# Kernel tuning notes

Measured on AMD Instinct MI355X. Metric: run time of the kernel, lower is better.

The kernel has to match this reference:

```python
import jax, jax.numpy as jnp
import numpy as np

B, S, DIM, H, FFN = 2, 2048, 1024, 16, 4096
HD = DIM // H
THETA = 10000.0
EPS = 1e-5


def setup_inputs() -> dict:
    key = jax.random.key(0)
    ks = jax.random.split(key, 12)
    s = 0.02
    return {
        "x": jax.random.normal(ks[0], (B, S, DIM), jnp.float32),
        "padding_mask": jnp.zeros((B, S), jnp.bool_),
        "qkv_w": jax.random.normal(ks[1], (DIM, 3 * DIM), jnp.float32) * s,
        "qkv_b": jnp.zeros((3 * DIM,), jnp.float32),
        "out_w": jax.random.normal(ks[2], (DIM, DIM), jnp.float32) * s,
        "out_b": jnp.zeros((DIM,), jnp.float32),
        "ln1_g": jnp.ones((DIM,), jnp.float32),
        "ln1_b": jnp.zeros((DIM,), jnp.float32),
        "ln2_g": jnp.ones((DIM,), jnp.float32),
        "ln2_b": jnp.zeros((DIM,), jnp.float32),
        "w1": jax.random.normal(ks[3], (DIM, FFN), jnp.float32) * s,
        "b1": jnp.zeros((FFN,), jnp.float32),
        "w2": jax.random.normal(ks[4], (FFN, DIM), jnp.float32) * s,
        "b2": jnp.zeros((DIM,), jnp.float32),
    }


def _layer_norm(x, g, b):
    mu = jnp.mean(x, axis=-1, keepdims=True)
    var = jnp.mean(jnp.square(x - mu), axis=-1, keepdims=True)
    return (x - mu) * jax.lax.rsqrt(var + EPS) * g + b


def _rotate_half(x):
    x1, x2 = jnp.split(x, 2, axis=-1)
    return jnp.concatenate([-x2, x1], axis=-1)


def reference(x, padding_mask, qkv_w, qkv_b, out_w, out_b,
              ln1_g, ln1_b, ln2_g, ln2_b, w1, b1, w2, b2):
    b, s, _ = x.shape
    residual = x
    h = _layer_norm(x, ln1_g, ln1_b)
    qkv = h @ qkv_w + qkv_b  # [b, s, 3*dim]
    q, k, v = jnp.split(qkv, 3, axis=-1)
    # [b, heads, s, head_dim]
    q = q.reshape(b, s, H, HD).transpose(0, 2, 1, 3)
    k = k.reshape(b, s, H, HD).transpose(0, 2, 1, 3)
    v = v.reshape(b, s, H, HD).transpose(0, 2, 1, 3)

    # rotary embeddings
    pos = jnp.arange(s, dtype=jnp.float32)
    inv_freq = 1.0 / (THETA ** (jnp.arange(0, HD, 2, dtype=jnp.float32) / HD))
    freqs = pos[:, None] * inv_freq[None, :]          # [s, hd/2]
    emb = jnp.concatenate([freqs, freqs], axis=-1)    # [s, hd]
    sin = jnp.sin(emb)[None, None, :, :]
    cos = jnp.cos(emb)[None, None, :, :]
    q = q * cos + _rotate_half(q) * sin
    k = k * cos + _rotate_half(k) * sin

    scale = HD ** (-0.5)
    scores = jnp.einsum('bhqd,bhkd->bhqk', q, k) * scale
    neg = jnp.finfo(scores.dtype).min
    scores = jnp.where(padding_mask[:, None, None, :], neg, scores)
    probs = jax.nn.softmax(scores, axis=-1)
    ctx = jnp.einsum('bhqk,bhkd->bhqd', probs, v)
    ctx = ctx.transpose(0, 2, 1, 3).reshape(b, s, DIM)
    x = residual + (ctx @ out_w + out_b)

    residual = x
    h = _layer_norm(x, ln2_g, ln2_b)
    h = jax.nn.gelu(h @ w1 + b1, approximate=False) @ w2 + b2
    return residual + h
```

## Files before the change

kernel.cpp:

```cpp
#include <hip/hip_runtime.h>
#include <hip/hip_bf16.h>
#include <math.h>

typedef __hip_bfloat16 bf16;
typedef __attribute__((ext_vector_type(8))) short short8;
typedef __attribute__((ext_vector_type(4))) float floatx4;

constexpr int BB   = 2;
constexpr int SS   = 2048;
constexpr int DIMc = 1024;
constexpr int Hc   = 16;
constexpr int HDc  = 64;
constexpr int FFNc = 4096;
constexpr int TOK  = BB * SS;
constexpr float EPSc = 1e-5f;

typedef __attribute__((address_space(1))) void gvoid;
typedef __attribute__((address_space(3))) void lvoid;
__device__ __forceinline__ void lds16(const void* g, void* l) {
    __builtin_amdgcn_global_load_lds((gvoid*)g, (lvoid*)l, 16, 0, 0);
}
__device__ __forceinline__ float fexp2(float x) { return __builtin_amdgcn_exp2f(x); }

__device__ __forceinline__ float fast_gelu(float x) {
    float x2 = x * x;
    float z = 0.7978845608028654f * x * __builtin_fmaf(0.044715f, x2, 1.0f);
    float e = fexp2(-2.885390081777927f * z);
    return x * __builtin_amdgcn_rcpf(1.0f + e);
}

__global__ __launch_bounds__(256) void ln_kernel(const float* __restrict__ x,
                                                 const float* __restrict__ g,
                                                 const float* __restrict__ b,
                                                 bf16* __restrict__ out) {
    int t = blockIdx.x;
    int tid = threadIdx.x;
    float4 v = ((const float4*)(x + (size_t)t * DIMc))[tid];
    float s  = v.x + v.y + v.z + v.w;
    float sq = v.x*v.x + v.y*v.y + v.z*v.z + v.w*v.w;
    for (int off = 1; off < 64; off <<= 1) {
        s  += __shfl_xor(s,  off, 64);
        sq += __shfl_xor(sq, off, 64);
    }
    __shared__ float ss[4], ssq[4];
    int wave = tid >> 6;
    if ((tid & 63) == 0) { ss[wave] = s; ssq[wave] = sq; }
    __syncthreads();
    s  = ss[0] + ss[1] + ss[2] + ss[3];
    sq = ssq[0] + ssq[1] + ssq[2] + ssq[3];
    float mu  = s * (1.0f / DIMc);
    float var = sq * (1.0f / DIMc) - mu * mu;
    float inv = rsqrtf(var + EPSc);
    float4 gg = ((const float4*)g)[tid];
    float4 bb = ((const float4*)b)[tid];
    size_t base = (size_t)t * DIMc + tid * 4;
    out[base + 0] = __float2bfloat16((v.x - mu) * inv * gg.x + bb.x);
    out[base + 1] = __float2bfloat16((v.y - mu) * inv * gg.y + bb.y);
    out[base + 2] = __float2bfloat16((v.z - mu) * inv * gg.z + bb.z);
    out[base + 3] = __float2bfloat16((v.w - mu) * inv * gg.w + bb.w);
}

__global__ __launch_bounds__(256) void reduce_ln_kernel(const float* __restrict__ P,
                                                        const float* __restrict__ x,
                                                        const float* __restrict__ bias,
                                                        const float* __restrict__ g,
                                                        const float* __restrict__ b,
                                                        float* __restrict__ out,
                                                        bf16* __restrict__ hout) {
    int t = blockIdx.x;
    int tid = threadIdx.x;
    size_t off = (size_t)t * DIMc / 4 + tid;
    float4 v  = ((const float4*)x)[off];
    float4 p0 = ((const float4*)P)[off];
    float4 p1 = ((const float4*)P)[off + (size_t)TOK * DIMc / 4];
    float4 bv = ((const float4*)bias)[tid];
    v.x += p0.x + p1.x + bv.x;
    v.y += p0.y + p1.y + bv.y;
    v.z += p0.z + p1.z + bv.z;
    v.w += p0.w + p1.w + bv.w;
    ((float4*)out)[off] = v;

    float s  = v.x + v.y + v.z + v.w;
    float sq = v.x*v.x + v.y*v.y + v.z*v.z + v.w*v.w;
    for (int o = 1; o < 64; o <<= 1) {
        s  += __shfl_xor(s,  o, 64);
        sq += __shfl_xor(sq, o, 64);
    }
    __shared__ float ss[4], ssq[4];
    int wave = tid >> 6;
    if ((tid & 63) == 0) { ss[wave] = s; ssq[wave] = sq; }
    __syncthreads();
    s  = ss[0] + ss[1] + ss[2] + ss[3];
    sq = ssq[0] + ssq[1] + ssq[2] + ssq[3];
    float mu  = s * (1.0f / DIMc);
    float var = sq * (1.0f / DIMc) - mu * mu;
    float inv = rsqrtf(var + EPSc);
    float4 gg = ((const float4*)g)[tid];
    float4 bb = ((const float4*)b)[tid];
    size_t base = (size_t)t * DIMc + tid * 4;
    hout[base + 0] = __float2bfloat16((v.x - mu) * inv * gg.x + bb.x);
    hout[base + 1] = __float2bfloat16((v.y - mu) * inv * gg.y + bb.y);
    hout[base + 2] = __float2bfloat16((v.z - mu) * inv * gg.z + bb.z);
    hout[base + 3] = __float2bfloat16((v.w - mu) * inv * gg.w + bb.w);
}

__global__ __launch_bounds__(256) void reduce_add_kernel(const float* __restrict__ P,
                                                         const float* __restrict__ bias,
                                                         float* __restrict__ out) {
    size_t f = (size_t)blockIdx.x * 256 + threadIdx.x;
    float4 v  = ((float4*)out)[f];
    float4 p0 = ((const float4*)P)[f];
    float4 p1 = ((const float4*)P)[f + (size_t)TOK * DIMc / 4];
    float4 bv = ((const float4*)bias)[f & (DIMc / 4 - 1)];
    v.x += p0.x + p1.x + bv.x;
    v.y += p0.y + p1.y + bv.y;
    v.z += p0.z + p1.z + bv.z;
    v.w += p0.w + p1.w + bv.w;
    ((float4*)out)[f] = v;
}

__global__ __launch_bounds__(256) void transpose_bf16(const float* __restrict__ in,
                                                      bf16* __restrict__ out,
                                                      int K, int N) {
    __shared__ float t[32][33];
    int k0 = blockIdx.y * 32, n0 = blockIdx.x * 32;
    int x = threadIdx.x & 31;
    int y = threadIdx.x >> 5;
#pragma unroll
    for (int i = 0; i < 4; ++i) {
        int k = y + i * 8;
        t[k][x] = in[(size_t)(k0 + k) * N + n0 + x];
    }
    __syncthreads();
#pragma unroll
    for (int i = 0; i < 4; ++i) {
        int n = y + i * 8;
        out[(size_t)(n0 + n) * K + k0 + x] = __float2bfloat16(t[x][n]);
    }
}

__global__ __launch_bounds__(256) void transpose_v(const bf16* __restrict__ qkv,
                                                   bf16* __restrict__ vT) {
    __shared__ short t[64][72];
    const int s0 = blockIdx.x * 64, h = blockIdx.y, b = blockIdx.z;
    const int tid = threadIdx.x;
    const short* qs = (const short*)qkv;
#pragma unroll
    for (int it = 0; it < 2; ++it) {
        int idx = it * 256 + tid;
        int r = idx >> 3, c = (idx & 7) * 8;
        *(short8*)&t[r][c] = *(const short8*)(qs + (size_t)(b * SS + s0 + r) * 3072
                                              + 2048 + h * 64 + c);
    }
    __syncthreads();
#pragma unroll
    for (int it = 0; it < 2; ++it) {
        int idx = it * 256 + tid;
        int d = idx >> 3, cs = (idx & 7) * 8;
        short8 v;
#pragma unroll
        for (int j = 0; j < 8; ++j) v[j] = t[cs + j][d];
        *(short8*)((short*)vT + ((size_t)(b * Hc + h) * 64 + d) * SS + s0 + cs) = v;
    }
}

__device__ __forceinline__ void xcd_remap(int& bx, int& by) {
    const int gn = gridDim.x;
    int lin = blockIdx.y * gn + blockIdx.x;
    int k8 = lin & 7, idx = lin >> 3;
    int hn = gn >> 1;
    by = (k8 >> 1) * 8 + (idx & 7);
    bx = (k8 & 1) * hn + (idx >> 3);
}

template <int ACT, bool ROPE>
__global__ __launch_bounds__(256) void gemm_bt(const bf16* __restrict__ A,
                                               const bf16* __restrict__ Bt,
                                               const float* __restrict__ bias,
                                               bf16* __restrict__ Cout,
                                               int M, int N, int K) {
    constexpr int BK = 64;
    __shared__ bf16 As[2][128 * 32];
    __shared__ bf16 Bs[2][128 * 32];
    const int tid = threadIdx.x;
    const int wave = tid >> 6, lane = tid & 63;
    const int lane15 = lane & 15, lgrp = lane >> 4;
    const int wm = (wave >> 1) * 64, wn = (wave & 1) * 64;
    int bx, by; xcd_remap(bx, by);
    const int row0 = by * 128, col0 = bx * 128;

    floatx4 acc[4][4] = {};

    const int srow = wave * 16 + (lane >> 2);
    const int scol = (((lane & 3) + (srow >> 1)) & 3) * 8;
    const bf16* ga = A  + (size_t)(row0 + srow) * K + scol;
    const bf16* gb = Bt + (size_t)(col0 + srow) * K + scol;
    const int g_l = (lgrp - (lane15 >> 1)) & 3;

    for (int k0 = 0; k0 < K; k0 += BK) {
        __syncthreads();
#pragma unroll
        for (int p = 0; p < 4; ++p) {
            const size_t go = (size_t)((p & 1) * 64) * K + k0 + (p >> 1) * 32;
            lds16(ga + go, &As[p >> 1][(p & 1) * 2048 + wave * 512]);
            lds16(gb + go, &Bs[p >> 1][(p & 1) * 2048 + wave * 512]);
        }
        __syncthreads();
#pragma unroll
        for (int s = 0; s < 2; ++s) {
            short8 af[4], bfr[4];
#pragma unroll
            for (int i = 0; i < 4; ++i)
                af[i] = *(const short8*)(&As[s][(wm + i * 16 + lane15) * 32 + g_l * 8]);
#pragma unroll
            for (int j = 0; j < 4; ++j)
                bfr[j] = *(const short8*)(&Bs[s][(wn + j * 16 + lane15) * 32 + g_l * 8]);
#pragma unroll
            for (int i = 0; i < 4; ++i)
#pragma unroll
                for (int j = 0; j < 4; ++j)
                    acc[i][j] = __builtin_amdgcn_mfma_f32_16x16x32_bf16(af[i], bfr[j], acc[i][j], 0, 0, 0);
        }
    }

    const bool doRope = ROPE && (col0 < 2048);
    float invf0 = 0.f, invf1 = 0.f;
    if (ROPE) {
        invf0 = fexp2(-0.4152410118609203f * (float)lane15);
        invf1 = fexp2(-0.4152410118609203f * (float)(16 + lane15));
    }
    float bv[4];
#pragma unroll
    for (int j = 0; j < 4; ++j) bv[j] = bias[col0 + wn + j * 16 + lane15];

#pragma unroll
    for (int i = 0; i < 4; ++i) {
#pragma unroll
        for (int r = 0; r < 4; ++r) {
            int row = row0 + wm + i * 16 + lgrp * 4 + r;
            float v[4];
#pragma unroll
            for (int j = 0; j < 4; ++j) v[j] = acc[i][j][r] + bv[j];
            if (doRope) {
                float pos = (float)(row & (SS - 1));
                float s0, c0, s1, c1;
                __sincosf(pos * invf0, &s0, &c0);
                __sincosf(pos * invf1, &s1, &c1);
                float t0 = v[0] * c0 - v[2] * s0;
                float t1 = v[1] * c1 - v[3] * s1;
                float t2 = v[2] * c0 + v[0] * s0;
                float t3 = v[3] * c1 + v[1] * s1;
                v[0] = t0; v[1] = t1; v[2] = t2; v[3] = t3;
            }
#pragma unroll
            for (int j = 0; j < 4; ++j) {
                float o = v[j];
                if (ACT == 1) o = fast_gelu(o);
                Cout[(size_t)row * N + col0 + wn + j * 16 + lane15] = __float2bfloat16(o);
            }
        }
    }
}

__global__ __launch_bounds__(256) void gemm_bt_splitk(const bf16* __restrict__ A,
                                                      const bf16* __restrict__ Bt,
                                                      float* __restrict__ P,
                                                      int M, int N, int K, int KCH) {
    constexpr int BK = 64;
    __shared__ bf16 As[2][128 * 32];
    __shared__ bf16 Bs[2][128 * 32];
    const int tid = threadIdx.x;
    const int wave = tid >> 6, lane = tid & 63;
    const int lane15 = lane & 15, lgrp = lane >> 4;
    const int wm = (wave >> 1) * 64, wn = (wave & 1) * 64;
    int bx, by; xcd_remap(bx, by);
    const int row0 = by * 128, col0 = bx * 128;
    const int kbase = blockIdx.z * KCH;
    float* Cp = P + (size_t)blockIdx.z * M * N;

    floatx4 acc[4][4] = {};

    const int srow = wave * 16 + (lane >> 2);
    const int scol = (((lane & 3) + (srow >> 1)) & 3) * 8;
    const bf16* ga = A  + (size_t)(row0 + srow) * K + scol;
    const bf16* gb = Bt + (size_t)(col0 + srow) * K + scol;
    const int g_l = (lgrp - (lane15 >> 1)) & 3;

    for (int k0 = kbase; k0 < kbase + KCH; k0 += BK) {
        __syncthreads();
#pragma unroll
        for (int p = 0; p < 4; ++p) {
            const size_t go = (size_t)((p & 1) * 64) * K + k0 + (p >> 1) * 32;
            lds16(ga + go, &As[p >> 1][(p & 1) * 2048 + wave * 512]);
            lds16(gb + go, &Bs[p >> 1][(p & 1) * 2048 + wave * 512]);
        }
        __syncthreads();
#pragma unroll
        for (int s = 0; s < 2; ++s) {
            short8 af[4], bfr[4];
#pragma unroll
            for (int i = 0; i < 4; ++i)
                af[i] = *(const short8*)(&As[s][(wm + i * 16 + lane15) * 32 + g_l * 8]);
#pragma unroll
            for (int j = 0; j < 4; ++j)
                bfr[j] = *(const short8*)(&Bs[s][(wn + j * 16 + lane15) * 32 + g_l * 8]);
#pragma unroll
            for (int i = 0; i < 4; ++i)
#pragma unroll
                for (int j = 0; j < 4; ++j)
                    acc[i][j] = __builtin_amdgcn_mfma_f32_16x16x32_bf16(af[i], bfr[j], acc[i][j], 0, 0, 0);
        }
    }

#pragma unroll
    for (int i = 0; i < 4; ++i)
#pragma unroll
        for (int j = 0; j < 4; ++j) {
            int col = col0 + wn + j * 16 + lane15;
#pragma unroll
            for (int r = 0; r < 4; ++r) {
                int row = row0 + wm + i * 16 + lgrp * 4 + r;
                Cp[(size_t)row * N + col] = acc[i][j][r];
            }
        }
}

__global__ __launch_bounds__(256) void attn_mfma(const bf16* __restrict__ qkv,
                                                 const bf16* __restrict__ vT,
                                                 const unsigned char* __restrict__ mask,
                                                 float* __restrict__ Op,
                                                 float* __restrict__ Lp) {
    __shared__ short Klds[2][64][32];
    __shared__ short Vlds[2][64][32];
    __shared__ short Ps[4][32][72];
    __shared__ float mkf[64];

    const int h = blockIdx.y;
    const int b = blockIdx.z >> 1, kc = blockIdx.z & 1;
    const int q0 = blockIdx.x * 128;
    const int tid = threadIdx.x;
    const int wave = tid >> 6, lane = tid & 63;
    const int lane15 = lane & 15, lgrp = lane >> 4;
    const short* qs = (const short*)qkv;
    const short* vs = (const short*)vT + (size_t)(b * Hc + h) * 64 * SS;
    const int g_l = (lgrp - (lane15 >> 1)) & 3;

    short* qstage = &Ps[wave][0][0];
#pragma unroll
    for (int i = 0; i < 4; ++i) {
        int idx = i * 64 + lane;
        int g = idx & 3, row = (idx >> 2) & 15, s = (idx >> 6) & 1, mi = idx >> 7;
        const short* gq = qs + (size_t)(b * SS + q0 + wave * 32 + mi * 16 + row) * 3072
                             + h * 64 + s * 32 + g * 8;
        lds16(gq, qstage + idx * 8);
    }
    __syncthreads();
    short8 aQ[2][2];
#pragma unroll
    for (int mi = 0; mi < 2; ++mi)
#pragma unroll
        for (int s = 0; s < 2; ++s)
            aQ[mi][s] = *(const short8*)(qstage + ((mi * 2 + s) * 16 + lane15) * 32 + lgrp * 8);

    const short8 bOnes = (short8)(short)0x3F80;
    floatx4 O[2][4] = {};
    floatx4 Lacc[2] = {};
    const float cscale = 0.18033688011112042f;

    for (int t = 0; t < 16; ++t) {
        const int k0 = kc * 1024 + t * 64;
        __syncthreads();
#pragma unroll
        for (int i = 0; i < 2; ++i) {
            int idx = wave * 128 + i * 64 + lane;
            int g = idx & 3, row = (idx >> 2) & 63, s = idx >> 8;
            int gsw = (g + (row >> 1)) & 3;
            const short* gk = qs + (size_t)(b * SS + k0 + row) * 3072 + 1024
                                 + h * 64 + s * 32 + gsw * 8;
            lds16(gk, &Klds[0][0][0] + idx * 8);
        }
#pragma unroll
        for (int i = 0; i < 2; ++i) {
            int idx = wave * 128 + i * 64 + lane;
            int g = idx & 3, drow = (idx >> 2) & 63, s = idx >> 8;
            int gsw = (g + (drow >> 1)) & 3;
            const short* gv = vs + (size_t)drow * SS + k0 + s * 32 + gsw * 8;
            lds16(gv, &Vlds[0][0][0] + idx * 8);
        }
        if (tid < 16) {
            const unsigned char* mp = mask + b * SS + k0 + tid * 4;
#pragma unroll
            for (int j = 0; j < 4; ++j) mkf[tid * 4 + j] = mp[j] ? -1e30f : 0.0f;
        }
        __syncthreads();

        short8 bK[4][2];
#pragma unroll
        for (int j = 0; j < 4; ++j)
#pragma unroll
            for (int s = 0; s < 2; ++s)
                bK[j][s] = *(const short8*)&Klds[s][j * 16 + lane15][g_l * 8];
        floatx4 Sf[2][4] = {};
#pragma unroll
        for (int mi = 0; mi < 2; ++mi)
#pragma unroll
            for (int j = 0; j < 4; ++j)
#pragma unroll
                for (int s = 0; s < 2; ++s)
                    Sf[mi][j] = __builtin_amdgcn_mfma_f32_16x16x32_bf16(aQ[mi][s], bK[j][s], Sf[mi][j], 0, 0, 0);

        float mkv[4];
#pragma unroll
        for (int j = 0; j < 4; ++j) mkv[j] = mkf[j * 16 + lane15];

#pragma unroll
        for (int mi = 0; mi < 2; ++mi)
#pragma unroll
            for (int r = 0; r < 4; ++r)
#pragma unroll
                for (int j = 0; j < 4; ++j) {
                    float p = fexp2(Sf[mi][j][r] * cscale + mkv[j]);
                    bf16 tt = __float2bfloat16(p);
                    Ps[wave][mi * 16 + lgrp * 4 + r][lane15 + 16 * j] = *(short*)&tt;
                }

        short8 aP[2][2], bV[4][2];
#pragma unroll
        for (int mi = 0; mi < 2; ++mi)
#pragma unroll
            for (int s = 0; s < 2; ++s)
                aP[mi][s] = *(const short8*)&Ps[wave][mi * 16 + lane15][s * 32 + lgrp * 8];
#pragma unroll
        for (int jd = 0; jd < 4; ++jd)
#pragma unroll
            for (int s = 0; s < 2; ++s)
                bV[jd][s] = *(const short8*)&Vlds[s][jd * 16 + lane15][g_l * 8];
#pragma unroll
        for (int mi = 0; mi < 2; ++mi) {
#pragma unroll
            for (int jd = 0; jd < 4; ++jd)
#pragma unroll
                for (int s = 0; s < 2; ++s)
                    O[mi][jd] = __builtin_amdgcn_mfma_f32_16x16x32_bf16(aP[mi][s], bV[jd][s], O[mi][jd], 0, 0, 0);
#pragma unroll
            for (int s = 0; s < 2; ++s)
                Lacc[mi] = __builtin_amdgcn_mfma_f32_16x16x32_bf16(aP[mi][s], bOnes, Lacc[mi], 0, 0, 0);
        }
    }

    float* myOp = Op + (size_t)kc * TOK * DIMc;
#pragma unroll
    for (int mi = 0; mi < 2; ++mi)
#pragma unroll
        for (int r = 0; r < 4; ++r) {
            int q = q0 + wave * 32 + mi * 16 + lgrp * 4 + r;
            size_t rowoff = (size_t)(b * SS + q) * DIMc + h * 64 + lane15;
#pragma unroll
            for (int jd = 0; jd < 4; ++jd)
                myOp[rowoff + jd * 16] = O[mi][jd][r];
            if (lane15 == 0)
                Lp[((size_t)kc * TOK + b * SS + q) * Hc + h] = Lacc[mi][r];
        }
}

__global__ __launch_bounds__(256) void attn_combine(const float* __restrict__ Op,
                                                    const float* __restrict__ Lp,
                                                    bf16* __restrict__ ctx) {
    int t = blockIdx.x;
    int tid = threadIdx.x;
    int h = tid >> 4;
    size_t f = (size_t)t * (DIMc / 4) + tid;
    float4 p0 = ((const float4*)Op)[f];
    float4 p1 = ((const float4*)Op)[f + (size_t)TOK * DIMc / 4];
    float inv = 1.0f / (Lp[(size_t)t * Hc + h] + Lp[((size_t)TOK + t) * Hc + h]);
    size_t base = (size_t)t * DIMc + tid * 4;
    ctx[base + 0] = __float2bfloat16((p0.x + p1.x) * inv);
    ctx[base + 1] = __float2bfloat16((p0.y + p1.y) * inv);
    ctx[base + 2] = __float2bfloat16((p0.z + p1.z) * inv);
    ctx[base + 3] = __float2bfloat16((p0.w + p1.w) * inv);
}

extern "C" void kernel_launch(void* const* d_in, const int* in_sizes, int n_in,
                              void* d_out, int out_size, void* d_ws, size_t ws_size,
                              hipStream_t stream) {
    const float* x      = (const float*)d_in[0];
    const unsigned char* pmask = (const unsigned char*)d_in[1];
    const float* qkv_w  = (const float*)d_in[2];
    const float* qkv_b  = (const float*)d_in[3];
    const float* out_w  = (const float*)d_in[4];
    const float* out_b  = (const float*)d_in[5];
    const float* ln1_g  = (const float*)d_in[6];
    const float* ln1_b  = (const float*)d_in[7];
    const float* ln2_g  = (const float*)d_in[8];
    const float* ln2_b  = (const float*)d_in[9];
    const float* w1     = (const float*)d_in[10];
    const float* b1     = (const float*)d_in[11];
    const float* w2     = (const float*)d_in[12];
    const float* b2     = (const float*)d_in[13];
    float* out = (float*)d_out;

    char* ws = (char*)d_ws;
    bf16* wqkv_t = (bf16*)ws;                      ws += (size_t)3072 * 1024 * 2;
    bf16* wout_t = (bf16*)ws;                      ws += (size_t)1024 * 1024 * 2;
    bf16* w1_t   = (bf16*)ws;                      ws += (size_t)4096 * 1024 * 2;
    bf16* w2_t   = (bf16*)ws;                      ws += (size_t)1024 * 4096 * 2;
    bf16* h_bf   = (bf16*)ws;                      ws += (size_t)TOK * DIMc * 2;
    bf16* qkv_bf = (bf16*)ws;                      ws += (size_t)TOK * 3 * DIMc * 2;
    bf16* ctx_bf = (bf16*)ws;                      ws += (size_t)TOK * DIMc * 2;
    float* partial = (float*)ws;                   ws += (size_t)2 * TOK * DIMc * 4;
    float* Lp      = (float*)ws;                   ws += (size_t)2 * TOK * Hc * 4;
    bf16* ffn1_bf = qkv_bf;
    bf16* vT      = h_bf;

    transpose_bf16<<<dim3(3072 / 32, 1024 / 32), 256, 0, stream>>>(qkv_w, wqkv_t, 1024, 3072);
    transpose_bf16<<<dim3(1024 / 32, 1024 / 32), 256, 0, stream>>>(out_w, wout_t, 1024, 1024);
    transpose_bf16<<<dim3(4096 / 32, 1024 / 32), 256, 0, stream>>>(w1,    w1_t,   1024, 4096);
    transpose_bf16<<<dim3(1024 / 32, 4096 / 32), 256, 0, stream>>>(w2,    w2_t,   4096, 1024);

    ln_kernel<<<TOK, 256, 0, stream>>>(x, ln1_g, ln1_b, h_bf);
    gemm_bt<0, true><<<dim3(3072 / 128, TOK / 128), 256, 0, stream>>>(
        h_bf, wqkv_t, qkv_b, qkv_bf, TOK, 3 * DIMc, DIMc);
    transpose_v<<<dim3(SS / 64, Hc, BB), 256, 0, stream>>>(qkv_bf, vT);
    attn_mfma<<<dim3(SS / 128, Hc, BB * 2), 256, 0, stream>>>(qkv_bf, vT, pmask, partial, Lp);
    attn_combine<<<TOK, 256, 0, stream>>>(partial, Lp, ctx_bf);

    gemm_bt_splitk<<<dim3(1024 / 128, TOK / 128, 2), 256, 0, stream>>>(
        ctx_bf, wout_t, partial, TOK, DIMc, DIMc, 512);
    reduce_ln_kernel<<<TOK, 256, 0, stream>>>(partial, x, out_b, ln2_g, ln2_b, out, h_bf);

    gemm_bt<1, false><<<dim3(4096 / 128, TOK / 128), 256, 0, stream>>>(
        h_bf, w1_t, b1, ffn1_bf, TOK, FFNc, DIMc);
    gemm_bt_splitk<<<dim3(1024 / 128, TOK / 128, 2), 256, 0, stream>>>(
        ffn1_bf, w2_t, partial, TOK, DIMc, FFNc, 2048);
    reduce_add_kernel<<<TOK * DIMc / 4 / 256, 256, 0, stream>>>(partial, b2, out);
}
```

Measured before the change: 371.1 us.

## Double attention key tile per sync and remap block indices for L2 locality

The attention kernel now loads 128 keys per iteration (two 64-key halves) into larger LDS buffers and processes both halves between barriers, halving the number of __syncthreads and global-to-LDS rounds. Block indices are also flattened and remapped so that consecutive blocks share the same query tile across heads, batches and key chunks, which changes the L2 access pattern. This costs more LDS per block, which may reduce occupancy, and Ps is still reused per wave within an iteration without an extra barrier.

```diff
diff --git a/kernel.cpp b/kernel.cpp
--- a/kernel.cpp
+++ b/kernel.cpp
@@ -330,14 +330,16 @@
                                                  const unsigned char* __restrict__ mask,
                                                  float* __restrict__ Op,
                                                  float* __restrict__ Lp) {
-    __shared__ short Klds[2][64][32];
-    __shared__ short Vlds[2][64][32];
+    __shared__ short Klds[4][64][32];
+    __shared__ short Vlds[4][64][32];
     __shared__ short Ps[4][32][72];
-    __shared__ float mkf[64];
-
-    const int h = blockIdx.y;
-    const int b = blockIdx.z >> 1, kc = blockIdx.z & 1;
-    const int q0 = blockIdx.x * 128;
+    __shared__ float mkf[128];
+
+    const int f = blockIdx.x + 16 * blockIdx.y + 256 * blockIdx.z;
+    const int c = f & 63, qi = f >> 6;
+    const int kc = c & 1, h = (c >> 1) & 15, b = c >> 5;
+    const int q0 = qi * 128;
+
     const int tid = threadIdx.x;
     const int wave = tid >> 6, lane = tid & 63;
     const int lane15 = lane & 15, lgrp = lane >> 4;
@@ -367,84 +369,89 @@
     floatx4 Lacc[2] = {};
     const float cscale = 0.18033688011112042f;
 
-    for (int t = 0; t < 16; ++t) {
-        const int k0 = kc * 1024 + t * 64;
+    for (int t = 0; t < 8; ++t) {
+        const int k0 = kc * 1024 + t * 128;
         __syncthreads();
 #pragma unroll
-        for (int i = 0; i < 2; ++i) {
-            int idx = wave * 128 + i * 64 + lane;
-            int g = idx & 3, row = (idx >> 2) & 63, s = idx >> 8;
-            int gsw = (g + (row >> 1)) & 3;
-            const short* gk = qs + (size_t)(b * SS + k0 + row) * 3072 + 1024
-                                 + h * 64 + s * 32 + gsw * 8;
+        for (int i = 0; i < 4; ++i) {
+            int idx = wave * 256 + i * 64 + lane;
+            int g = idx & 3, key63 = (idx >> 2) & 63, sh = (idx >> 8) & 1, kh = idx >> 9;
+            int gsw = (g + (key63 >> 1)) & 3;
+            const short* gk = qs + (size_t)(b * SS + k0 + kh * 64 + key63) * 3072 + 1024
+                                 + h * 64 + sh * 32 + gsw * 8;
             lds16(gk, &Klds[0][0][0] + idx * 8);
         }
 #pragma unroll
-        for (int i = 0; i < 2; ++i) {
-            int idx = wave * 128 + i * 64 + lane;
-            int g = idx & 3, drow = (idx >> 2) & 63, s = idx >> 8;
-            int gsw = (g + (drow >> 1)) & 3;
-            const short* gv = vs + (size_t)drow * SS + k0 + s * 32 + gsw * 8;
+        for (int i = 0; i < 4; ++i) {
+            int idx = wave * 256 + i * 64 + lane;
+            int g = idx & 3, d = (idx >> 2) & 63, sh = (idx >> 8) & 1, kh = idx >> 9;
+            int gsw = (g + (d >> 1)) & 3;
+            const short* gv = vs + (size_t)d * SS + k0 + kh * 64 + sh * 32 + gsw * 8;
             lds16(gv, &Vlds[0][0][0] + idx * 8);
         }
-        if (tid < 16) {
+        if (tid < 32) {
             const unsigned char* mp = mask + b * SS + k0 + tid * 4;
 #pragma unroll
             for (int j = 0; j < 4; ++j) mkf[tid * 4 + j] = mp[j] ? -1e30f : 0.0f;
         }
         __syncthreads();
 
-        short8 bK[4][2];
-#pragma unroll
-        for (int j = 0; j < 4; ++j)
-#pragma unroll
-            for (int s = 0; s < 2; ++s)
-                bK[j][s] = *(const short8*)&Klds[s][j * 16 + lane15][g_l * 8];
-        floatx4 Sf[2][4] = {};
-#pragma unroll
-        for (int mi = 0; mi < 2; ++mi)
+#pragma unroll
+        for (int kh = 0; kh < 2; ++kh) {
+            short8 bK[4][2];
 #pragma unroll
             for (int j = 0; j < 4; ++j)
 #pragma unroll
                 for (int s = 0; s < 2; ++s)
-                    Sf[mi][j] = __builtin_amdgcn_mfma_f32_16x16x32_bf16(aQ[mi][s], bK[j][s], Sf[mi][j], 0, 0, 0);
-
-        float mkv[4];
-#pragma unroll
-        for (int j = 0; j < 4; ++j) mkv[j] = mkf[j * 16 + lane15];
-
-#pragma unroll
-        for (int mi = 0; mi < 2; ++mi)
-#pragma unroll
-            for (int r = 0; r < 4; ++r)
-#pragma unroll
-                for (int j = 0; j < 4; ++j) {
-                    float p = fexp2(Sf[mi][j][r] * cscale + mkv[j]);
-                    bf16 tt = __float2bfloat16(p);
-                    Ps[wave][mi * 16 + lgrp * 4 + r][lane15 + 16 * j] = *(short*)&tt;
-                }
-
-        short8 aP[2][2], bV[4][2];
-#pragma unroll
-        for (int mi = 0; mi < 2; ++mi)
-#pragma unroll
-            for (int s = 0; s < 2; ++s)
-                aP[mi][s] = *(const short8*)&Ps[wave][mi * 16 + lane15][s * 32 + lgrp * 8];
-#pragma unroll
-        for (int jd = 0; jd < 4; ++jd)
-#pragma unroll
-            for (int s = 0; s < 2; ++s)
-                bV[jd][s] = *(const short8*)&Vlds[s][jd * 16 + lane15][g_l * 8];
-#pragma unroll
-        for (int mi = 0; mi < 2; ++mi) {
+                    bK[j][s] = *(const short8*)(&Klds[0][0][0]
+                               + ((kh * 2 + s) * 64 + j * 16 + lane15) * 32 + g_l * 8);
+            floatx4 Sf[2][4] = {};
+#pragma unroll
+            for (int mi = 0; mi < 2; ++mi)
+#pragma unroll
+                for (int j = 0; j < 4; ++j)
+#pragma unroll
+                    for (int s = 0; s < 2; ++s)
+                        Sf[mi][j] = __builtin_amdgcn_mfma_f32_16x16x32_bf16(aQ[mi][s], bK[j][s], Sf[mi][j], 0, 0, 0);
+
+            float mkv[4];
+#pragma unroll
+            for (int j = 0; j < 4; ++j) mkv[j] = mkf[kh * 64 + j * 16 + lane15];
+
+#pragma unroll
+            for (int mi = 0; mi < 2; ++mi)
+#pragma unroll
+                for (int r = 0; r < 4; ++r)
+#pragma unroll
+                    for (int j = 0; j < 4; ++j) {
+                        float p = fexp2(Sf[mi][j][r] * cscale + mkv[j]);
+                        bf16 tt = __float2bfloat16(p);
+                        Ps[wave][mi * 16 + lgrp * 4 + r][lane15 + 16 * j] = *(short*)&tt;
+                    }
+
+            short8 aP[2][2], bV[4][2];
+#pragma unroll
+            for (int mi = 0; mi < 2; ++mi)
+#pragma unroll
+                for (int s = 0; s < 2; ++s)
+                    aP[mi][s] = *(const short8*)&Ps[wave][mi * 16 + lane15][s * 32 + lgrp * 8];
 #pragma unroll
             for (int jd = 0; jd < 4; ++jd)
 #pragma unroll
                 for (int s = 0; s < 2; ++s)
-                    O[mi][jd] = __builtin_amdgcn_mfma_f32_16x16x32_bf16(aP[mi][s], bV[jd][s], O[mi][jd], 0, 0, 0);
-#pragma unroll
-            for (int s = 0; s < 2; ++s)
-                Lacc[mi] = __builtin_amdgcn_mfma_f32_16x16x32_bf16(aP[mi][s], bOnes, Lacc[mi], 0, 0, 0);
+                    bV[jd][s] = *(const short8*)(&Vlds[0][0][0]
+                                + ((kh * 2 + s) * 64 + jd * 16 + lane15) * 32 + g_l * 8);
+#pragma unroll
+            for (int mi = 0; mi < 2; ++mi) {
+#pragma unroll
+                for (int jd = 0; jd < 4; ++jd)
+#pragma unroll
+                    for (int s = 0; s < 2; ++s)
+                        O[mi][jd] = __builtin_amdgcn_mfma_f32_16x16x32_bf16(aP[mi][s], bV[jd][s], O[mi][jd], 0, 0, 0);
+#pragma unroll
+                for (int s = 0; s < 2; ++s)
+                    Lacc[mi] = __builtin_amdgcn_mfma_f32_16x16x32_bf16(aP[mi][s], bOnes, Lacc[mi], 0, 0, 0);
+            }
         }
     }
 
```

After: 390.2 us. 1.05x slower.
